# Optimization experiments

Measured on AMD Instinct MI355X. Metric: run time of the kernel, lower is better.

## Reference

```python
import jax, jax.numpy as jnp
import numpy as np

NODELEN = 10


def setup_inputs() -> dict:
    key = jax.random.key(0)
    ks = jax.random.split(key, 16)
    N, DEG = 200000, 32
    IN, H1, H2, EMB = 2 * NODELEN, 15, 10, 5
    features = jax.random.normal(ks[0], (N, NODELEN), dtype=jnp.float32)
    adj = jax.random.randint(ks[1], (N, DEG), 0, N, dtype=jnp.int32)
    s = 0.1
    inp = {
        'features': features,
        'adj': adj,
        'We1': jax.random.normal(ks[2], (H1, IN), dtype=jnp.float32) * s,
        'be1': jnp.zeros((H1,), dtype=jnp.float32),
        'We2': jax.random.normal(ks[3], (H2, H1), dtype=jnp.float32) * s,
        'be2': jnp.zeros((H2,), dtype=jnp.float32),
        'We3': jax.random.normal(ks[4], (EMB, H2), dtype=jnp.float32) * s,
        'be3': jnp.zeros((EMB,), dtype=jnp.float32),
        'Wd1': jax.random.normal(ks[5], (H2, EMB), dtype=jnp.float32) * s,
        'bd1': jnp.zeros((H2,), dtype=jnp.float32),
        'Wd2': jax.random.normal(ks[6], (H1, H2), dtype=jnp.float32) * s,
        'bd2': jnp.zeros((H1,), dtype=jnp.float32),
        'Wd3': jax.random.normal(ks[7], (IN, H1), dtype=jnp.float32) * s,
        'bd3': jnp.zeros((IN,), dtype=jnp.float32),
    }
    return inp


def _autoencoder(x, We1, be1, We2, be2, We3, be3, Wd1, bd1, Wd2, bd2, Wd3, bd3):
    # torch nn.Linear: y = x @ W.T + b ; dropout is identity in eval
    h = jax.nn.relu(x @ We1.T + be1)
    h = jax.nn.relu(h @ We2.T + be2)
    encoded = h @ We3.T + be3
    h = jax.nn.relu(encoded @ Wd1.T + bd1)
    h = jax.nn.relu(h @ Wd2.T + bd2)
    decoded = h @ Wd3.T + bd3
    return encoded, decoded


def reference(features, adj, We1, be1, We2, be2, We3, be3,
              Wd1, bd1, Wd2, bd2, Wd3, bd3):
    # depth-2 recursive neighbor aggregation (aggregate_neighbors):
    # hop 1: mean of raw neighbor features, element 0 zeroed
    h1 = jnp.mean(features[adj], axis=1)          # [N, deg, F] -> [N, F]
    h1 = h1.at[:, 0].set(0.0)
    # hop 2: mean of hop-1 features of neighbors, element 0 zeroed
    agg = jnp.mean(h1[adj], axis=1)
    agg = agg.at[:, 0].set(0.0)
    # generate_embedding: concat(self, aggregated), zero positions 0 and NODELEN
    emb = jnp.concatenate([features, agg], axis=1)
    emb = emb.at[:, 0].set(0.0).at[:, NODELEN].set(0.0)
    encoded, decoded = _autoencoder(emb, We1, be1, We2, be2, We3, be3,
                                    Wd1, bd1, Wd2, bd2, Wd3, bd3)
    return encoded, decoded, emb
```

## Files before the change

kernel.cpp:

```cpp
#include <hip/hip_runtime.h>

#define NODELEN 10
#define DEG 32


#if defined(__has_builtin)
#if __has_builtin(__builtin_amdgcn_cvt_pk_f32_fp8)
#define USE_HW_FP8_DECODE 1
#endif
#endif

typedef float floatx2 __attribute__((ext_vector_type(2)));

__device__ __forceinline__ float fp8_to_f32_sw(unsigned b) {
    unsigned s = (b & 0x80u) << 24;
    unsigned e = (b >> 3) & 0xFu;
    unsigned m = b & 0x7u;
    float fn = __uint_as_float(s | ((e + 120u) << 23) | (m << 20));
    float fs = __uint_as_float(s | __float_as_uint((float)m * 0.001953125f));
    return e ? fn : fs;
}

__device__ __forceinline__ void dacc(float& a, float& b, unsigned w, int hi) {
#if defined(USE_HW_FP8_DECODE)
    floatx2 f = hi ? __builtin_amdgcn_cvt_pk_f32_fp8(w, true)
                   : __builtin_amdgcn_cvt_pk_f32_fp8(w, false);
    a += f.x; b += f.y;
#else
    unsigned p = hi ? (w >> 16) : w;
    a += fp8_to_f32_sw(p & 0xFFu);
    b += fp8_to_f32_sw((p >> 8) & 0xFFu);
#endif
}

__device__ __forceinline__ unsigned fp8_encode(float f) {
    unsigned u = __float_as_uint(f);
    unsigned s = u >> 31;
    float a = fabsf(f);
    if (a < 0.015625f) {
        int mi = __float2int_rn(a * 512.0f);
        return (s << 7) | (unsigned)mi;
    }
    int e = (int)((u >> 23) & 0xFFu) - 127;
    unsigned mant = u & 0x7FFFFFu;
    unsigned r = mant + 0x7FFFFu + ((mant >> 20) & 1u);
    mant = r >> 20;
    if (mant == 8u) { mant = 0u; e += 1; }
    return (s << 7) | ((unsigned)(e + 7) << 3) | mant;
}

__device__ __forceinline__ int4 pack_row_fp8(const float* v) {
    unsigned b[NODELEN];
#pragma unroll
    for (int k = 0; k < NODELEN; ++k) b[k] = fp8_encode(v[k]);
    int4 p;
    p.x = (int)(b[0] | (b[1] << 8) | (b[2] << 16) | (b[3] << 24));
    p.y = (int)(b[4] | (b[5] << 8) | (b[6] << 16) | (b[7] << 24));
    p.z = (int)(b[8] | (b[9] << 8));
    p.w = 0;
    return p;
}

__device__ __forceinline__ void row_acc(float* s, int4 p) {
    unsigned w0 = (unsigned)p.x, w1 = (unsigned)p.y, w2 = (unsigned)p.z;
    dacc(s[0], s[1], w0, 0);
    dacc(s[2], s[3], w0, 1);
    dacc(s[4], s[5], w1, 0);
    dacc(s[6], s[7], w1, 1);
    dacc(s[8], s[9], w2, 0);
}

__global__ __launch_bounds__(256) void prep_kernel(
    const float* __restrict__ features,
    int4*        __restrict__ f8feat,
    int N)
{
    int i = blockIdx.x * blockDim.x + threadIdx.x;
    if (i >= N) return;
    const float2* r = (const float2*)(features + (size_t)i * NODELEN);
    float2 a0 = r[0], a1 = r[1], a2 = r[2], a3 = r[3], a4 = r[4];
    float v[NODELEN] = {a0.x, a0.y, a1.x, a1.y, a2.x, a2.y, a3.x, a3.y, a4.x, a4.y};
    f8feat[i] = pack_row_fp8(v);
}

__global__ __launch_bounds__(256) void hop1_kernel(
    const int4* __restrict__ f8feat,
    const int*  __restrict__ adj,
    int4*       __restrict__ f8h1,
    int N)
{
    int i = blockIdx.x * blockDim.x + threadIdx.x;
    if (i >= N) return;

    const int4* arow = (const int4*)(adj + (size_t)i * DEG);

    float s[NODELEN];
#pragma unroll
    for (int k = 0; k < NODELEN; ++k) s[k] = 0.0f;

#pragma unroll
    for (int j = 0; j < DEG / 4; ++j) {
        int4 nb = arow[j];
        row_acc(s, f8feat[nb.x]);
        row_acc(s, f8feat[nb.y]);
        row_acc(s, f8feat[nb.z]);
        row_acc(s, f8feat[nb.w]);
    }

    const float inv = 1.0f / (float)DEG;
    float h[NODELEN];
    h[0] = 0.0f;
#pragma unroll
    for (int k = 1; k < NODELEN; ++k) h[k] = s[k] * inv;
    f8h1[i] = pack_row_fp8(h);
}

__global__ __launch_bounds__(256) void hop2_mlp_kernel(
    const float* __restrict__ features,
    const int*   __restrict__ adj,
    const int4*  __restrict__ f8h1,
    const float* __restrict__ We1, const float* __restrict__ be1,
    const float* __restrict__ We2, const float* __restrict__ be2,
    const float* __restrict__ We3, const float* __restrict__ be3,
    const float* __restrict__ Wd1, const float* __restrict__ bd1,
    const float* __restrict__ Wd2, const float* __restrict__ bd2,
    const float* __restrict__ Wd3, const float* __restrict__ bd3,
    float* __restrict__ out_enc,
    float* __restrict__ out_dec,
    float* __restrict__ out_emb,
    int N)
{
    int i = blockIdx.x * blockDim.x + threadIdx.x;
    if (i >= N) return;

    const int4* arow = (const int4*)(adj + (size_t)i * DEG);

    float s[NODELEN];
#pragma unroll
    for (int k = 0; k < NODELEN; ++k) s[k] = 0.0f;

#pragma unroll
    for (int j = 0; j < DEG / 4; ++j) {
        int4 nb = arow[j];
        row_acc(s, f8h1[nb.x]);
        row_acc(s, f8h1[nb.y]);
        row_acc(s, f8h1[nb.z]);
        row_acc(s, f8h1[nb.w]);
    }

    const float inv = 1.0f / (float)DEG;

    const float2* fr = (const float2*)(features + (size_t)i * NODELEN);
    float2 f0 = fr[0], f1 = fr[1], f2 = fr[2], f3 = fr[3], f4 = fr[4];

    float emb[2 * NODELEN];
    emb[0] = 0.0f;  emb[1] = f0.y;
    emb[2] = f1.x;  emb[3] = f1.y;
    emb[4] = f2.x;  emb[5] = f2.y;
    emb[6] = f3.x;  emb[7] = f3.y;
    emb[8] = f4.x;  emb[9] = f4.y;
    emb[10] = 0.0f;
#pragma unroll
    for (int k = 1; k < NODELEN; ++k) emb[10 + k] = s[k] * inv;

    float t1[15];
#pragma unroll
    for (int o = 0; o < 15; ++o) {
        float acc = be1[o];
#pragma unroll
        for (int k = 0; k < 20; ++k) acc = fmaf(We1[o * 20 + k], emb[k], acc);
        t1[o] = fmaxf(acc, 0.0f);
    }
    float t2[10];
#pragma unroll
    for (int o = 0; o < 10; ++o) {
        float acc = be2[o];
#pragma unroll
        for (int k = 0; k < 15; ++k) acc = fmaf(We2[o * 15 + k], t1[k], acc);
        t2[o] = fmaxf(acc, 0.0f);
    }
    float enc[5];
#pragma unroll
    for (int o = 0; o < 5; ++o) {
        float acc = be3[o];
#pragma unroll
        for (int k = 0; k < 10; ++k) acc = fmaf(We3[o * 10 + k], t2[k], acc);
        enc[o] = acc;
    }
    float t3[10];
#pragma unroll
    for (int o = 0; o < 10; ++o) {
        float acc = bd1[o];
#pragma unroll
        for (int k = 0; k < 5; ++k) acc = fmaf(Wd1[o * 5 + k], enc[k], acc);
        t3[o] = fmaxf(acc, 0.0f);
    }
    float t4[15];
#pragma unroll
    for (int o = 0; o < 15; ++o) {
        float acc = bd2[o];
#pragma unroll
        for (int k = 0; k < 10; ++k) acc = fmaf(Wd2[o * 10 + k], t3[k], acc);
        t4[o] = fmaxf(acc, 0.0f);
    }
    float dec[20];
#pragma unroll
    for (int o = 0; o < 20; ++o) {
        float acc = bd3[o];
#pragma unroll
        for (int k = 0; k < 15; ++k) acc = fmaf(Wd3[o * 15 + k], t4[k], acc);
        dec[o] = acc;
    }

    float* pe = out_enc + (size_t)i * 5;
    pe[0] = enc[0]; pe[1] = enc[1]; pe[2] = enc[2]; pe[3] = enc[3]; pe[4] = enc[4];

    float4* pd = (float4*)(out_dec + (size_t)i * 20);
    pd[0] = make_float4(dec[0],  dec[1],  dec[2],  dec[3]);
    pd[1] = make_float4(dec[4],  dec[5],  dec[6],  dec[7]);
    pd[2] = make_float4(dec[8],  dec[9],  dec[10], dec[11]);
    pd[3] = make_float4(dec[12], dec[13], dec[14], dec[15]);
    pd[4] = make_float4(dec[16], dec[17], dec[18], dec[19]);

    float4* pm = (float4*)(out_emb + (size_t)i * 20);
    pm[0] = make_float4(emb[0],  emb[1],  emb[2],  emb[3]);
    pm[1] = make_float4(emb[4],  emb[5],  emb[6],  emb[7]);
    pm[2] = make_float4(emb[8],  emb[9],  emb[10], emb[11]);
    pm[3] = make_float4(emb[12], emb[13], emb[14], emb[15]);
    pm[4] = make_float4(emb[16], emb[17], emb[18], emb[19]);
}

extern "C" void kernel_launch(void* const* d_in, const int* in_sizes, int n_in,
                              void* d_out, int out_size, void* d_ws, size_t ws_size,
                              hipStream_t stream)
{
    const float* features = (const float*)d_in[0];
    const int*   adj      = (const int*)  d_in[1];
    const float* We1 = (const float*)d_in[2];  const float* be1 = (const float*)d_in[3];
    const float* We2 = (const float*)d_in[4];  const float* be2 = (const float*)d_in[5];
    const float* We3 = (const float*)d_in[6];  const float* be3 = (const float*)d_in[7];
    const float* Wd1 = (const float*)d_in[8];  const float* bd1 = (const float*)d_in[9];
    const float* Wd2 = (const float*)d_in[10]; const float* bd2 = (const float*)d_in[11];
    const float* Wd3 = (const float*)d_in[12]; const float* bd3 = (const float*)d_in[13];

    const int N = in_sizes[0] / NODELEN;

    int4* f8feat = (int4*)d_ws;
    int4* f8h1   = (int4*)((char*)d_ws + (size_t)N * 16);

    float* out     = (float*)d_out;
    float* out_enc = out;
    float* out_dec = out + (size_t)N * 5;
    float* out_emb = out + (size_t)N * 25;

    const int threads = 256;
    const int blocks  = (N + threads - 1) / threads;

    hipLaunchKernelGGL(prep_kernel, dim3(blocks), dim3(threads), 0, stream,
                       features, f8feat, N);
    hipLaunchKernelGGL(hop1_kernel, dim3(blocks), dim3(threads), 0, stream,
                       f8feat, adj, f8h1, N);
    hipLaunchKernelGGL(hop2_mlp_kernel, dim3(blocks), dim3(threads), 0, stream,
                       features, adj, f8h1,
                       We1, be1, We2, be2, We3, be3,
                       Wd1, bd1, Wd2, bd2, Wd3, bd3,
                       out_enc, out_dec, out_emb, N);
}
```

Measured before the change: 206.4 us.

## Split neighbor gathers across four lanes per node and stage outputs through LDS

Both hop kernels now assign four threads per node, each gathering 8 of the 32 neighbors, and combine the partial sums with xor shuffles. This adds memory-level parallelism and makes each thread's adjacency read contiguous. The hop2 kernel also stages features and the enc/dec/emb outputs through shared memory so global reads and writes are coalesced float4 accesses. The trade-off is that the MLP now runs on only 64 of 256 threads per block, and the extra barriers and shuffles add overhead.

```diff
diff --git a/kernel.cpp b/kernel.cpp
--- a/kernel.cpp
+++ b/kernel.cpp
@@ -2,6 +2,7 @@
 
 #define NODELEN 10
 #define DEG 32
+#define NPB 64
 
 
 #if defined(__has_builtin)
@@ -89,30 +90,39 @@
     int4*       __restrict__ f8h1,
     int N)
 {
-    int i = blockIdx.x * blockDim.x + threadIdx.x;
+    int t = blockIdx.x * blockDim.x + threadIdx.x;
+    int i = t >> 2, sub = t & 3;
     if (i >= N) return;
 
-    const int4* arow = (const int4*)(adj + (size_t)i * DEG);
+    const int4* arow = (const int4*)(adj + (size_t)i * DEG + sub * 8);
+    int4 n0 = arow[0], n1 = arow[1];
 
     float s[NODELEN];
 #pragma unroll
     for (int k = 0; k < NODELEN; ++k) s[k] = 0.0f;
-
-#pragma unroll
-    for (int j = 0; j < DEG / 4; ++j) {
-        int4 nb = arow[j];
-        row_acc(s, f8feat[nb.x]);
-        row_acc(s, f8feat[nb.y]);
-        row_acc(s, f8feat[nb.z]);
-        row_acc(s, f8feat[nb.w]);
-    }
-
-    const float inv = 1.0f / (float)DEG;
-    float h[NODELEN];
-    h[0] = 0.0f;
-#pragma unroll
-    for (int k = 1; k < NODELEN; ++k) h[k] = s[k] * inv;
-    f8h1[i] = pack_row_fp8(h);
+    row_acc(s, f8feat[n0.x]);
+    row_acc(s, f8feat[n0.y]);
+    row_acc(s, f8feat[n0.z]);
+    row_acc(s, f8feat[n0.w]);
+    row_acc(s, f8feat[n1.x]);
+    row_acc(s, f8feat[n1.y]);
+    row_acc(s, f8feat[n1.z]);
+    row_acc(s, f8feat[n1.w]);
+
+#pragma unroll
+    for (int k = 0; k < NODELEN; ++k) {
+        s[k] += __shfl_xor(s[k], 1);
+        s[k] += __shfl_xor(s[k], 2);
+    }
+
+    if (sub == 0) {
+        const float inv = 1.0f / (float)DEG;
+        float h[NODELEN];
+        h[0] = 0.0f;
+#pragma unroll
+        for (int k = 1; k < NODELEN; ++k) h[k] = s[k] * inv;
+        f8h1[i] = pack_row_fp8(h);
+    }
 }
 
 __global__ __launch_bounds__(256) void hop2_mlp_kernel(
@@ -130,104 +140,147 @@
     float* __restrict__ out_emb,
     int N)
 {
-    int i = blockIdx.x * blockDim.x + threadIdx.x;
-    if (i >= N) return;
-
-    const int4* arow = (const int4*)(adj + (size_t)i * DEG);
+    __shared__ float  s_agg[NPB][11];
+    __shared__ float4 s_feat4[NPB * 10 / 4];
+    __shared__ float4 s_enc4[NPB * 5 / 4];
+    __shared__ float4 s_dec4[NPB * 20 / 4];
+    __shared__ float4 s_emb4[NPB * 20 / 4];
+
+    const int tid  = threadIdx.x;
+    const int base = blockIdx.x * NPB;
+    const int nl   = tid >> 2, sub = tid & 3;
+    const int i    = base + nl;
+    const bool full = (base + NPB <= N);
+
+    if (full) {
+        const float4* gf = (const float4*)(features + (size_t)base * NODELEN);
+        if (tid < NPB * 10 / 4) s_feat4[tid] = gf[tid];
+    } else {
+        int cnt = (N - base) * NODELEN;
+        for (int k = tid; k < cnt; k += 256)
+            ((float*)s_feat4)[k] = features[(size_t)base * NODELEN + k];
+    }
 
     float s[NODELEN];
 #pragma unroll
     for (int k = 0; k < NODELEN; ++k) s[k] = 0.0f;
-
-#pragma unroll
-    for (int j = 0; j < DEG / 4; ++j) {
-        int4 nb = arow[j];
-        row_acc(s, f8h1[nb.x]);
-        row_acc(s, f8h1[nb.y]);
-        row_acc(s, f8h1[nb.z]);
-        row_acc(s, f8h1[nb.w]);
-    }
-
-    const float inv = 1.0f / (float)DEG;
-
-    const float2* fr = (const float2*)(features + (size_t)i * NODELEN);
-    float2 f0 = fr[0], f1 = fr[1], f2 = fr[2], f3 = fr[3], f4 = fr[4];
-
-    float emb[2 * NODELEN];
-    emb[0] = 0.0f;  emb[1] = f0.y;
-    emb[2] = f1.x;  emb[3] = f1.y;
-    emb[4] = f2.x;  emb[5] = f2.y;
-    emb[6] = f3.x;  emb[7] = f3.y;
-    emb[8] = f4.x;  emb[9] = f4.y;
-    emb[10] = 0.0f;
-#pragma unroll
-    for (int k = 1; k < NODELEN; ++k) emb[10 + k] = s[k] * inv;
-
-    float t1[15];
-#pragma unroll
-    for (int o = 0; o < 15; ++o) {
-        float acc = be1[o];
-#pragma unroll
-        for (int k = 0; k < 20; ++k) acc = fmaf(We1[o * 20 + k], emb[k], acc);
-        t1[o] = fmaxf(acc, 0.0f);
-    }
-    float t2[10];
-#pragma unroll
-    for (int o = 0; o < 10; ++o) {
-        float acc = be2[o];
-#pragma unroll
-        for (int k = 0; k < 15; ++k) acc = fmaf(We2[o * 15 + k], t1[k], acc);
-        t2[o] = fmaxf(acc, 0.0f);
-    }
-    float enc[5];
-#pragma unroll
-    for (int o = 0; o < 5; ++o) {
-        float acc = be3[o];
-#pragma unroll
-        for (int k = 0; k < 10; ++k) acc = fmaf(We3[o * 10 + k], t2[k], acc);
-        enc[o] = acc;
-    }
-    float t3[10];
-#pragma unroll
-    for (int o = 0; o < 10; ++o) {
-        float acc = bd1[o];
-#pragma unroll
-        for (int k = 0; k < 5; ++k) acc = fmaf(Wd1[o * 5 + k], enc[k], acc);
-        t3[o] = fmaxf(acc, 0.0f);
-    }
-    float t4[15];
-#pragma unroll
-    for (int o = 0; o < 15; ++o) {
-        float acc = bd2[o];
-#pragma unroll
-        for (int k = 0; k < 10; ++k) acc = fmaf(Wd2[o * 10 + k], t3[k], acc);
-        t4[o] = fmaxf(acc, 0.0f);
-    }
-    float dec[20];
-#pragma unroll
-    for (int o = 0; o < 20; ++o) {
-        float acc = bd3[o];
-#pragma unroll
-        for (int k = 0; k < 15; ++k) acc = fmaf(Wd3[o * 15 + k], t4[k], acc);
-        dec[o] = acc;
-    }
-
-    float* pe = out_enc + (size_t)i * 5;
-    pe[0] = enc[0]; pe[1] = enc[1]; pe[2] = enc[2]; pe[3] = enc[3]; pe[4] = enc[4];
-
-    float4* pd = (float4*)(out_dec + (size_t)i * 20);
-    pd[0] = make_float4(dec[0],  dec[1],  dec[2],  dec[3]);
-    pd[1] = make_float4(dec[4],  dec[5],  dec[6],  dec[7]);
-    pd[2] = make_float4(dec[8],  dec[9],  dec[10], dec[11]);
-    pd[3] = make_float4(dec[12], dec[13], dec[14], dec[15]);
-    pd[4] = make_float4(dec[16], dec[17], dec[18], dec[19]);
-
-    float4* pm = (float4*)(out_emb + (size_t)i * 20);
-    pm[0] = make_float4(emb[0],  emb[1],  emb[2],  emb[3]);
-    pm[1] = make_float4(emb[4],  emb[5],  emb[6],  emb[7]);
-    pm[2] = make_float4(emb[8],  emb[9],  emb[10], emb[11]);
-    pm[3] = make_float4(emb[12], emb[13], emb[14], emb[15]);
-    pm[4] = make_float4(emb[16], emb[17], emb[18], emb[19]);
+    if (i < N) {
+        const int4* arow = (const int4*)(adj + (size_t)i * DEG + sub * 8);
+        int4 n0 = arow[0], n1 = arow[1];
+        row_acc(s, f8h1[n0.x]);
+        row_acc(s, f8h1[n0.y]);
+        row_acc(s, f8h1[n0.z]);
+        row_acc(s, f8h1[n0.w]);
+        row_acc(s, f8h1[n1.x]);
+        row_acc(s, f8h1[n1.y]);
+        row_acc(s, f8h1[n1.z]);
+        row_acc(s, f8h1[n1.w]);
+    }
+#pragma unroll
+    for (int k = 0; k < NODELEN; ++k) {
+        s[k] += __shfl_xor(s[k], 1);
+        s[k] += __shfl_xor(s[k], 2);
+    }
+    if (sub == 0 && i < N) {
+#pragma unroll
+        for (int k = 0; k < NODELEN; ++k) s_agg[nl][k] = s[k];
+    }
+    __syncthreads();
+
+    if (tid < NPB) {
+        int node = base + tid;
+        if (node < N) {
+            const float inv = 1.0f / (float)DEG;
+            const float* fr = (const float*)s_feat4 + tid * NODELEN;
+
+            float emb[2 * NODELEN];
+            emb[0] = 0.0f;
+#pragma unroll
+            for (int k = 1; k < NODELEN; ++k) emb[k] = fr[k];
+            emb[NODELEN] = 0.0f;
+#pragma unroll
+            for (int k = 1; k < NODELEN; ++k) emb[NODELEN + k] = s_agg[tid][k] * inv;
+
+            float t1[15];
+#pragma unroll
+            for (int o = 0; o < 15; ++o) {
+                float acc = be1[o];
+#pragma unroll
+                for (int k = 0; k < 20; ++k) acc = fmaf(We1[o * 20 + k], emb[k], acc);
+                t1[o] = fmaxf(acc, 0.0f);
+            }
+            float t2[10];
+#pragma unroll
+            for (int o = 0; o < 10; ++o) {
+                float acc = be2[o];
+#pragma unroll
+                for (int k = 0; k < 15; ++k) acc = fmaf(We2[o * 15 + k], t1[k], acc);
+                t2[o] = fmaxf(acc, 0.0f);
+            }
+            float enc[5];
+#pragma unroll
+            for (int o = 0; o < 5; ++o) {
+                float acc = be3[o];
+#pragma unroll
+                for (int k = 0; k < 10; ++k) acc = fmaf(We3[o * 10 + k], t2[k], acc);
+                enc[o] = acc;
+            }
+            float t3[10];
+#pragma unroll
+            for (int o = 0; o < 10; ++o) {
+                float acc = bd1[o];
+#pragma unroll
+                for (int k = 0; k < 5; ++k) acc = fmaf(Wd1[o * 5 + k], enc[k], acc);
+                t3[o] = fmaxf(acc, 0.0f);
+            }
+            float t4[15];
+#pragma unroll
+            for (int o = 0; o < 15; ++o) {
+                float acc = bd2[o];
+#pragma unroll
+                for (int k = 0; k < 10; ++k) acc = fmaf(Wd2[o * 10 + k], t3[k], acc);
+                t4[o] = fmaxf(acc, 0.0f);
+            }
+            float dec[20];
+#pragma unroll
+            for (int o = 0; o < 20; ++o) {
+                float acc = bd3[o];
+#pragma unroll
+                for (int k = 0; k < 15; ++k) acc = fmaf(Wd3[o * 15 + k], t4[k], acc);
+                dec[o] = acc;
+            }
+
+            float* se = (float*)s_enc4;
+#pragma unroll
+            for (int k = 0; k < 5; ++k) se[tid * 5 + k] = enc[k];
+            float* sd = (float*)s_dec4;
+#pragma unroll
+            for (int k = 0; k < 20; ++k) sd[tid * 20 + k] = dec[k];
+            float* sm = (float*)s_emb4;
+#pragma unroll
+            for (int k = 0; k < 20; ++k) sm[tid * 20 + k] = emb[k];
+        }
+    }
+    __syncthreads();
+
+    if (full) {
+        float4* gd = (float4*)(out_dec + (size_t)base * 20);
+#pragma unroll
+        for (int k = tid; k < NPB * 20 / 4; k += 256) gd[k] = s_dec4[k];
+        float4* gm = (float4*)(out_emb + (size_t)base * 20);
+#pragma unroll
+        for (int k = tid; k < NPB * 20 / 4; k += 256) gm[k] = s_emb4[k];
+        float4* ge = (float4*)(out_enc + (size_t)base * 5);
+        if (tid < NPB * 5 / 4) ge[tid] = s_enc4[tid];
+    } else {
+        int cnt = N - base;
+        for (int k = tid; k < cnt * 20; k += 256)
+            out_dec[(size_t)base * 20 + k] = ((float*)s_dec4)[k];
+        for (int k = tid; k < cnt * 20; k += 256)
+            out_emb[(size_t)base * 20 + k] = ((float*)s_emb4)[k];
+        for (int k = tid; k < cnt * 5; k += 256)
+            out_enc[(size_t)base * 5 + k] = ((float*)s_enc4)[k];
+    }
 }
 
 extern "C" void kernel_launch(void* const* d_in, const int* in_sizes, int n_in,
@@ -254,13 +307,12 @@
     float* out_emb = out + (size_t)N * 25;
 
     const int threads = 256;
-    const int blocks  = (N + threads - 1) / threads;
-
-    hipLaunchKernelGGL(prep_kernel, dim3(blocks), dim3(threads), 0, stream,
+
+    hipLaunchKernelGGL(prep_kernel, dim3((N + 255) / 256), dim3(threads), 0, stream,
                        features, f8feat, N);
-    hipLaunchKernelGGL(hop1_kernel, dim3(blocks), dim3(threads), 0, stream,
+    hipLaunchKernelGGL(hop1_kernel, dim3((4 * N + 255) / 256), dim3(threads), 0, stream,
                        f8feat, adj, f8h1, N);
-    hipLaunchKernelGGL(hop2_mlp_kernel, dim3(blocks), dim3(threads), 0, stream,
+    hipLaunchKernelGGL(hop2_mlp_kernel, dim3((N + NPB - 1) / NPB), dim3(threads), 0, stream,
                        features, adj, f8h1,
                        We1, be1, We2, be2, We3, be3,
                        Wd1, bd1, Wd2, bd2, Wd3, bd3,
```

Result: faster. 181.8 us (-11.9%).
